# Optimization experiments

Hardware: AMD Instinct MI355X
Metric: run time of the kernel (lower is better)

Reference implementation:

```python
import jax, jax.numpy as jnp
import numpy as np

B, H, V, A, NANN, DEPTH = 32, 256, 512, 3, 8, 7


def preorder_perm(arity, depth):
    # level-order node index -> pre-order position permutation for a full arity-ary tree
    starts = np.cumsum([0] + [arity ** l for l in range(depth + 1)])
    order = []
    def rec(l, p):
        order.append(int(starts[l] + p))
        if l < depth:
            for c in range(arity):
                rec(l + 1, p * arity + c)
    rec(0, 0)
    return np.asarray(order, dtype=np.int32)


def setup_inputs() -> dict:
    key = jax.random.key(0)
    ks = jax.random.split(key, 12)
    s = 0.05
    return {
        "root_hiddens": jax.random.normal(ks[0], (B, H), jnp.float32),
        "ann_table": jax.random.normal(ks[1], (NANN, H), jnp.float32),
        "w1": jax.random.normal(ks[2], (2 * H, H), jnp.float32) * s,
        "b1": jnp.zeros((2 * H,), jnp.float32),
        "w2": jax.random.normal(ks[3], (V, 2 * H), jnp.float32) * s,
        "b2": jnp.zeros((V,), jnp.float32),
        "gru_w_ih": jax.random.normal(ks[4], (A, 3 * H, H), jnp.float32) * s,
        "gru_w_hh": jax.random.normal(ks[5], (A, 3 * H, H), jnp.float32) * s,
        "gru_b_ih": jnp.zeros((A, 3 * H), jnp.float32),
        "gru_b_hh": jnp.zeros((A, 3 * H), jnp.float32),
        "ann_ids": jax.random.randint(ks[6], (B,), 0, NANN, jnp.int32),
        "depth": DEPTH,
    }


def _forward(root_hiddens, ann_table, w1, b1, w2, b2,
             gru_w_ih, gru_w_hh, gru_b_ih, gru_b_hh, ann_ids, depth):
    b, h = root_hiddens.shape
    arity = gru_w_ih.shape[0]
    x = ann_table[ann_ids]                                   # [B,H] annotation embedding (GRU input at every node)
    # input-side gates are constant across the whole tree: precompute once
    gx = jnp.einsum('bh,agh->bag', x, gru_w_ih) + gru_b_ih   # [B,A,3H]
    xr, xz, xn = jnp.split(gx, 3, axis=-1)                   # each [B,A,H]

    hid = root_hiddens[:, None, :]                           # [B,1,H]
    levels = [hid]
    for _ in range(depth):
        gh = jnp.einsum('bnh,agh->bnag', hid, gru_w_hh) + gru_b_hh  # [B,n,A,3H]
        hr, hz, hn = jnp.split(gh, 3, axis=-1)
        r = jax.nn.sigmoid(xr[:, None] + hr)
        z = jax.nn.sigmoid(xz[:, None] + hz)
        n = jnp.tanh(xn[:, None] + r * hn)
        new_h = (1.0 - z) * n + z * hid[:, :, None, :]       # [B,n,A,H]
        hid = new_h.reshape(b, -1, h)                        # child c of node p -> p*A+c
        levels.append(hid)

    all_h = jnp.concatenate(levels, axis=1)                  # [B,N,H] level-order
    mid = jax.nn.sigmoid(jnp.einsum('bnh,oh->bno', all_h, w1) + b1)
    prod = jnp.einsum('bno,vo->bnv', mid, w2) + b2           # [B,N,V]
    perm = jnp.asarray(preorder_perm(arity, depth))
    return jnp.transpose(prod[:, perm, :], (1, 0, 2))        # [N,B,V] (seq-first, like pad_sequence)


def reference(root_hiddens, ann_table, w1, b1, w2, b2,
              gru_w_ih, gru_w_hh, gru_b_ih, gru_b_hh, ann_ids, depth):
    return _forward(root_hiddens, ann_table, w1, b1, w2, b2,
                    gru_w_ih, gru_w_hh, gru_b_ih, gru_b_hh, ann_ids, depth)
```

## Files before the change

kernel.cpp:

```cpp
#include <hip/hip_runtime.h>
#include <hip/hip_bf16.h>
#include <stdint.h>
#include <stddef.h>

#define NB 32
#define NH 256
#define NMID 512
#define NV 512
#define NA 3
#define NDEPTH 7
#define NNODES 3280
#define NG 2304
#define MROWS (NNODES * NB)
#define HM 64

typedef __attribute__((ext_vector_type(8))) short bf16x8;
typedef __attribute__((ext_vector_type(4))) float f32x4;

__device__ __forceinline__ unsigned short f2bf(float x) {
    union { float f; unsigned u; } v; v.f = x;
    unsigned r = v.u + 0x7fffu + ((v.u >> 16) & 1u);
    return (unsigned short)(r >> 16);
}
__device__ __forceinline__ float bf2f(unsigned short u) {
    union { unsigned u; float f; } v; v.u = ((unsigned)u) << 16;
    return v.f;
}
__device__ __forceinline__ float sigm(float x) { return 1.0f / (1.0f + __expf(-x)); }
__device__ __forceinline__ float tanh_(float x) {
    x = fminf(fmaxf(x, -15.0f), 15.0f);
    float e = __expf(2.0f * x);
    return (e - 1.0f) / (e + 1.0f);
}
__device__ __forceinline__ f32x4 splat4(float s) { f32x4 v = {s, s, s, s}; return v; }

__global__ void cast_weights(const float* __restrict__ whh, const float* __restrict__ w1,
                             const float* __restrict__ w2,
                             unsigned short* __restrict__ whh_b,
                             unsigned short* __restrict__ w1_b,
                             unsigned short* __restrict__ w2_b) {
    const int n_whh = NG * NH;
    const int n_w1  = NMID * NH;
    const int n_w2  = NV * NMID;
    const int total = n_whh + n_w1 + n_w2;
    for (int i = blockIdx.x * blockDim.x + threadIdx.x; i < total;
         i += gridDim.x * blockDim.x) {
        if (i < n_whh) whh_b[i] = f2bf(whh[i]);
        else if (i < n_whh + n_w1) w1_b[i - n_whh] = f2bf(w1[i - n_whh]);
        else w2_b[i - n_whh - n_w1] = f2bf(w2[i - n_whh - n_w1]);
    }
}

__global__ void gx_kernel(const float* __restrict__ ann_table, const int* __restrict__ ann_ids,
                          const float* __restrict__ w_ih, const float* __restrict__ b_ih,
                          float* __restrict__ gx_t) {
    int gw = blockIdx.x * (blockDim.x >> 6) + (threadIdx.x >> 6);
    int lane = threadIdx.x & 63;
    if (gw >= NB * NG) return;
    int b = gw / NG;
    int col = gw - b * NG;
    const float* xr = ann_table + (size_t)ann_ids[b] * NH;
    const float* wr = w_ih + (size_t)col * NH;
    float4 xv = *(const float4*)(xr + lane * 4);
    float4 wv = *(const float4*)(wr + lane * 4);
    float s = xv.x * wv.x + xv.y * wv.y + xv.z * wv.z + xv.w * wv.w;
    #pragma unroll
    for (int off = 32; off; off >>= 1) s += __shfl_down(s, off);
    if (lane == 0) gx_t[(size_t)col * NB + b] = s + b_ih[col];
}

__global__ void init_root(const float* __restrict__ root, unsigned short* __restrict__ hid_b) {
    int i = blockIdx.x * blockDim.x + threadIdx.x;
    if (i < NB * NH) hid_b[i] = f2bf(root[i]);
}

__global__ void posmap_kernel(int* __restrict__ posmap) {
    int n = blockIdx.x * blockDim.x + threadIdx.x;
    if (n >= NNODES) return;
    int start = 0, cnt = 1, l = 0;
    while (n >= start + cnt) { start += cnt; cnt *= 3; l++; }
    int p = n - start;
    int pw = 1;
    for (int j = 0; j < l - 1; j++) pw *= 3;
    int pos = 0;
    for (int k = 1; k <= l; k++) {
        int d = (p / pw) % 3;
        int e = NDEPTH - k + 1;
        int p3 = 1; for (int j = 0; j < e; j++) p3 *= 3;
        pos += 1 + d * ((p3 - 1) / 2);
        pw /= 3;
    }
    posmap[n] = pos;
}

template<int NPB>
__global__ __launch_bounds__(512, 4)
void gru_level(const unsigned short* __restrict__ hid_b_in,
               unsigned short* __restrict__ hid_b_out,
               const unsigned short* __restrict__ whh_b,
               const float* __restrict__ b_hh, const float* __restrict__ gx_t,
               int start, int child_start, int cnt) {
    constexpr int M = 32 * NPB;
    __shared__ char a_s[M * 512];

    int tid = threadIdx.x;
    int lane = tid & 63;
    int wv = tid >> 6;
    int lr = lane & 15;
    int kg = (lane >> 4) * 8;
    int rbase = (lane >> 4) * 4;
    int nrel0 = blockIdx.x * NPB;
    size_t prow0 = (size_t)(start + nrel0) * NB;

    for (int c = tid; c < M * 32; c += 512) {
        int row = c >> 5;
        int coloff = (c & 31) * 8;
        bf16x8 v = *(const bf16x8*)(hid_b_in + (prow0 + row) * NH + coloff);
        *(bf16x8*)(a_s + ((row * 512 + coloff * 2) ^ ((row & 15) << 4))) = v;
    }
    __syncthreads();

    int Gb = (blockIdx.y * 8 + wv) * 16;
    int a = Gb >> 8;
    int colh = (Gb & 255) + lr;
    int gcol = a * 768 + colh;
    const unsigned short* bptr = whh_b + (size_t)(a * 512 + Gb + lr) * NH + kg;

    float bhr = b_hh[gcol], bhz = b_hh[gcol + 256], bhn = b_hh[gcol + 512];

    f32x4 acc[3][2 * NPB];
    #pragma unroll
    for (int g = 0; g < 2; ++g) {
        f32x4 gr = *(const f32x4*)(gx_t + (size_t)gcol * NB + g * 16 + rbase);
        f32x4 gz = *(const f32x4*)(gx_t + (size_t)(gcol + 256) * NB + g * 16 + rbase);
        #pragma unroll
        for (int mi = g; mi < 2 * NPB; mi += 2) {
            acc[0][mi] = gr + splat4(bhr);
            acc[1][mi] = gz + splat4(bhz);
            acc[2][mi] = splat4(bhn);
        }
    }

    bf16x8 bcur[3];
    #pragma unroll
    for (int t = 0; t < 3; ++t) bcur[t] = *(const bf16x8*)(bptr + t * 256 * NH);
    #pragma unroll
    for (int k0 = 0; k0 < NH; k0 += 32) {
        bf16x8 bnxt[3];
        if (k0 + 32 < NH) {
            #pragma unroll
            for (int t = 0; t < 3; ++t) bnxt[t] = *(const bf16x8*)(bptr + t * 256 * NH + k0 + 32);
        }
        bf16x8 af[2 * NPB];
        #pragma unroll
        for (int mi = 0; mi < 2 * NPB; ++mi) {
            int row = mi * 16 + lr;
            af[mi] = *(const bf16x8*)(a_s + ((row * 512 + (k0 + kg) * 2) ^ ((row & 15) << 4)));
        }
        #pragma unroll
        for (int t = 0; t < 3; ++t)
            #pragma unroll
            for (int mi = 0; mi < 2 * NPB; ++mi)
                acc[t][mi] = __builtin_amdgcn_mfma_f32_16x16x32_bf16(af[mi], bcur[t], acc[t][mi], 0, 0, 0);
        if (k0 + 32 < NH) {
            #pragma unroll
            for (int t = 0; t < 3; ++t) bcur[t] = bnxt[t];
        }
    }

    f32x4 gxn[2];
    #pragma unroll
    for (int g = 0; g < 2; ++g)
        gxn[g] = *(const f32x4*)(gx_t + (size_t)(gcol + 512) * NB + g * 16 + rbase);
    #pragma unroll
    for (int mi = 0; mi < 2 * NPB; ++mi) {
        #pragma unroll
        for (int j = 0; j < 4; ++j) {
            int row = mi * 16 + rbase + j;
            int ns = row >> 5;
            int b = row & 31;
            if (nrel0 + ns < cnt) {
                float r = sigm(acc[0][mi][j]);
                float z = sigm(acc[1][mi][j]);
                float nn = tanh_(gxn[mi & 1][j] + r * acc[2][mi][j]);
                unsigned short hpu = *(const unsigned short*)(a_s + ((row * 512 + colh * 2) ^ ((row & 15) << 4)));
                float hnew = (1.0f - z) * nn + z * bf2f(hpu);
                size_t crow = ((size_t)(child_start + (nrel0 + ns) * 3 + a)) * NB + b;
                hid_b_out[crow * NH + colh] = f2bf(hnew);
            }
        }
    }
}

__global__ __launch_bounds__(512, 4)
void head_fused(const unsigned short* __restrict__ hid_b,
                const unsigned short* __restrict__ w1_b, const float* __restrict__ b1,
                const unsigned short* __restrict__ w2_b, const float* __restrict__ b2,
                const int* __restrict__ posmap, float* __restrict__ out) {
    __shared__ char smem[HM * NMID * 2];

    int tid = threadIdx.x;
    int lane = tid & 63;
    int wv = tid >> 6;
    int mbase = blockIdx.x * HM;
    int lr = lane & 15;
    int kg = (lane >> 4) * 8;
    int rbase = (lane >> 4) * 4;
    int n0w = wv * 64;

    for (int c = tid; c < HM * 32; c += 512) {
        int row = c >> 5;
        int coloff = (c & 31) * 8;
        bf16x8 v = *(const bf16x8*)(hid_b + ((size_t)(mbase + row)) * NH + coloff);
        *(bf16x8*)(smem + ((row * 512 + coloff * 2) ^ ((row & 15) << 4))) = v;
    }
    __syncthreads();

    f32x4 acc[4][4];
    #pragma unroll
    for (int mi = 0; mi < 4; ++mi)
        #pragma unroll
        for (int ni = 0; ni < 4; ++ni) acc[mi][ni] = (f32x4){0.f, 0.f, 0.f, 0.f};

    {
        const unsigned short* bbase = w1_b + ((size_t)(n0w + lr)) * NH + kg;
        bf16x8 bcur[4];
        #pragma unroll
        for (int ni = 0; ni < 4; ++ni) bcur[ni] = *(const bf16x8*)(bbase + ni * 16 * NH);
        #pragma unroll
        for (int k0 = 0; k0 < NH; k0 += 32) {
            bf16x8 bnxt[4];
            if (k0 + 32 < NH) {
                #pragma unroll
                for (int ni = 0; ni < 4; ++ni) bnxt[ni] = *(const bf16x8*)(bbase + ni * 16 * NH + k0 + 32);
            }
            bf16x8 af[4];
            #pragma unroll
            for (int mi = 0; mi < 4; ++mi) {
                int row = mi * 16 + lr;
                af[mi] = *(const bf16x8*)(smem + ((row * 512 + (k0 + kg) * 2) ^ ((row & 15) << 4)));
            }
            #pragma unroll
            for (int mi = 0; mi < 4; ++mi)
                #pragma unroll
                for (int ni = 0; ni < 4; ++ni)
                    acc[mi][ni] = __builtin_amdgcn_mfma_f32_16x16x32_bf16(af[mi], bcur[ni], acc[mi][ni], 0, 0, 0);
            if (k0 + 32 < NH) {
                #pragma unroll
                for (int ni = 0; ni < 4; ++ni) bcur[ni] = bnxt[ni];
            }
        }
    }
    __syncthreads();

    #pragma unroll
    for (int mi = 0; mi < 4; ++mi)
        #pragma unroll
        for (int ni = 0; ni < 4; ++ni) {
            int col = n0w + ni * 16 + lr;
            float bv = b1[col];
            #pragma unroll
            for (int j = 0; j < 4; ++j) {
                int row = mi * 16 + rbase + j;
                float v = sigm(acc[mi][ni][j] + bv);
                *(unsigned short*)(smem + ((row * 1024 + col * 2) ^ ((row & 15) << 4))) = f2bf(v);
            }
        }
    __syncthreads();

    #pragma unroll
    for (int mi = 0; mi < 4; ++mi)
        #pragma unroll
        for (int ni = 0; ni < 4; ++ni) acc[mi][ni] = (f32x4){0.f, 0.f, 0.f, 0.f};
    {
        const unsigned short* bbase = w2_b + ((size_t)(n0w + lr)) * NMID + kg;
        bf16x8 bcur[4];
        #pragma unroll
        for (int ni = 0; ni < 4; ++ni) bcur[ni] = *(const bf16x8*)(bbase + ni * 16 * NMID);
        #pragma unroll
        for (int k0 = 0; k0 < NMID; k0 += 32) {
            bf16x8 bnxt[4];
            if (k0 + 32 < NMID) {
                #pragma unroll
                for (int ni = 0; ni < 4; ++ni) bnxt[ni] = *(const bf16x8*)(bbase + ni * 16 * NMID + k0 + 32);
            }
            bf16x8 af[4];
            #pragma unroll
            for (int mi = 0; mi < 4; ++mi) {
                int row = mi * 16 + lr;
                af[mi] = *(const bf16x8*)(smem + ((row * 1024 + (k0 + kg) * 2) ^ ((row & 15) << 4)));
            }
            #pragma unroll
            for (int mi = 0; mi < 4; ++mi)
                #pragma unroll
                for (int ni = 0; ni < 4; ++ni)
                    acc[mi][ni] = __builtin_amdgcn_mfma_f32_16x16x32_bf16(af[mi], bcur[ni], acc[mi][ni], 0, 0, 0);
            if (k0 + 32 < NMID) {
                #pragma unroll
                for (int ni = 0; ni < 4; ++ni) bcur[ni] = bnxt[ni];
            }
        }
    }
    #pragma unroll
    for (int mi = 0; mi < 4; ++mi)
        #pragma unroll
        for (int ni = 0; ni < 4; ++ni) {
            int col = n0w + ni * 16 + lr;
            float bv = b2[col];
            #pragma unroll
            for (int j = 0; j < 4; ++j) {
                int row = mbase + mi * 16 + rbase + j;
                int b = row & 31;
                int node = row >> 5;
                int pos = posmap[node];
                out[((size_t)pos * NB + b) * NV + col] = acc[mi][ni][j] + bv;
            }
        }
}

extern "C" void kernel_launch(void* const* d_in, const int* in_sizes, int n_in,
                              void* d_out, int out_size, void* d_ws, size_t ws_size,
                              hipStream_t stream) {
    const float* root      = (const float*)d_in[0];
    const float* ann_table = (const float*)d_in[1];
    const float* w1        = (const float*)d_in[2];
    const float* b1        = (const float*)d_in[3];
    const float* w2        = (const float*)d_in[4];
    const float* b2        = (const float*)d_in[5];
    const float* w_ih      = (const float*)d_in[6];
    const float* w_hh      = (const float*)d_in[7];
    const float* b_ih      = (const float*)d_in[8];
    const float* b_hh      = (const float*)d_in[9];
    const int*   ann_ids   = (const int*)d_in[10];

    uint8_t* ws = (uint8_t*)d_ws;
    unsigned short* whh_b = (unsigned short*)ws; ws += (size_t)NG * NH * 2;
    unsigned short* w1_b  = (unsigned short*)ws; ws += (size_t)NMID * NH * 2;
    unsigned short* w2_b  = (unsigned short*)ws; ws += (size_t)NV * NMID * 2;
    float* gx_t           = (float*)ws;          ws += (size_t)NB * NG * 4;
    int* posmap           = (int*)ws;            ws += (size_t)NNODES * 4;
    unsigned short* hid_b = (unsigned short*)ws; ws += (size_t)NNODES * NB * NH * 2;

    cast_weights<<<512, 256, 0, stream>>>(w_hh, w1, w2, whh_b, w1_b, w2_b);
    gx_kernel<<<(NB * NG) / 4, 256, 0, stream>>>(ann_table, ann_ids, w_ih, b_ih, gx_t);
    init_root<<<(NB * NH + 255) / 256, 256, 0, stream>>>(root, hid_b);
    posmap_kernel<<<(NNODES + 255) / 256, 256, 0, stream>>>(posmap);

    int start = 0, cnt = 1;
    for (int l = 0; l < NDEPTH; ++l) {
        int child_start = start + cnt;
        if (cnt >= 128) {
            gru_level<2><<<dim3((cnt + 1) / 2, 6), 512, 0, stream>>>(
                hid_b, hid_b, whh_b, b_hh, gx_t, start, child_start, cnt);
        } else {
            gru_level<1><<<dim3(cnt, 6), 512, 0, stream>>>(
                hid_b, hid_b, whh_b, b_hh, gx_t, start, child_start, cnt);
        }
        start = child_start; cnt *= 3;
    }
    head_fused<<<MROWS / HM, 512, 0, stream>>>(hid_b, w1_b, b1, w2_b, b2, posmap, (float*)d_out);
}
```

Before: 373.9 us.

## Shrink head tile to one node per block and retune GRU node batching

The head kernel now processes 32 rows (one tree node) per block instead of 64. That lets it look up posmap once per block and write contiguous output rows, and it drops the register double-buffering of weight fragments in favour of direct loads. Occupancy hints change (head 6, GRU 2), and large GRU levels batch 4 nodes per block starting from level size 243. The smaller head tile doubles weight-fragment global traffic per output row and loses software prefetch, in exchange for higher occupancy and cheaper output addressing.

```diff
diff --git a/kernel.cpp b/kernel.cpp
--- a/kernel.cpp
+++ b/kernel.cpp
@@ -12,7 +12,7 @@
 #define NNODES 3280
 #define NG 2304
 #define MROWS (NNODES * NB)
-#define HM 64
+#define HM 32
 
 typedef __attribute__((ext_vector_type(8))) short bf16x8;
 typedef __attribute__((ext_vector_type(4))) float f32x4;
@@ -94,7 +94,7 @@
 }
 
 template<int NPB>
-__global__ __launch_bounds__(512, 4)
+__global__ __launch_bounds__(512, 2)
 void gru_level(const unsigned short* __restrict__ hid_b_in,
                unsigned short* __restrict__ hid_b_out,
                const unsigned short* __restrict__ whh_b,
@@ -192,7 +192,7 @@
     }
 }
 
-__global__ __launch_bounds__(512, 4)
+__global__ __launch_bounds__(512, 6)
 void head_fused(const unsigned short* __restrict__ hid_b,
                 const unsigned short* __restrict__ w1_b, const float* __restrict__ b1,
                 const unsigned short* __restrict__ w2_b, const float* __restrict__ b2,
@@ -216,45 +216,35 @@
     }
     __syncthreads();
 
-    f32x4 acc[4][4];
-    #pragma unroll
-    for (int mi = 0; mi < 4; ++mi)
+    f32x4 acc[2][4];
+    #pragma unroll
+    for (int mi = 0; mi < 2; ++mi)
         #pragma unroll
         for (int ni = 0; ni < 4; ++ni) acc[mi][ni] = (f32x4){0.f, 0.f, 0.f, 0.f};
 
     {
         const unsigned short* bbase = w1_b + ((size_t)(n0w + lr)) * NH + kg;
-        bf16x8 bcur[4];
-        #pragma unroll
-        for (int ni = 0; ni < 4; ++ni) bcur[ni] = *(const bf16x8*)(bbase + ni * 16 * NH);
         #pragma unroll
         for (int k0 = 0; k0 < NH; k0 += 32) {
-            bf16x8 bnxt[4];
-            if (k0 + 32 < NH) {
-                #pragma unroll
-                for (int ni = 0; ni < 4; ++ni) bnxt[ni] = *(const bf16x8*)(bbase + ni * 16 * NH + k0 + 32);
-            }
-            bf16x8 af[4];
-            #pragma unroll
-            for (int mi = 0; mi < 4; ++mi) {
+            bf16x8 af[2], bfr[4];
+            #pragma unroll
+            for (int ni = 0; ni < 4; ++ni) bfr[ni] = *(const bf16x8*)(bbase + ni * 16 * NH + k0);
+            #pragma unroll
+            for (int mi = 0; mi < 2; ++mi) {
                 int row = mi * 16 + lr;
                 af[mi] = *(const bf16x8*)(smem + ((row * 512 + (k0 + kg) * 2) ^ ((row & 15) << 4)));
             }
             #pragma unroll
-            for (int mi = 0; mi < 4; ++mi)
+            for (int mi = 0; mi < 2; ++mi)
                 #pragma unroll
                 for (int ni = 0; ni < 4; ++ni)
-                    acc[mi][ni] = __builtin_amdgcn_mfma_f32_16x16x32_bf16(af[mi], bcur[ni], acc[mi][ni], 0, 0, 0);
-            if (k0 + 32 < NH) {
-                #pragma unroll
-                for (int ni = 0; ni < 4; ++ni) bcur[ni] = bnxt[ni];
-            }
+                    acc[mi][ni] = __builtin_amdgcn_mfma_f32_16x16x32_bf16(af[mi], bfr[ni], acc[mi][ni], 0, 0, 0);
         }
     }
     __syncthreads();
 
     #pragma unroll
-    for (int mi = 0; mi < 4; ++mi)
+    for (int mi = 0; mi < 2; ++mi)
         #pragma unroll
         for (int ni = 0; ni < 4; ++ni) {
             int col = n0w + ni * 16 + lr;
@@ -269,51 +259,40 @@
     __syncthreads();
 
     #pragma unroll
-    for (int mi = 0; mi < 4; ++mi)
+    for (int mi = 0; mi < 2; ++mi)
         #pragma unroll
         for (int ni = 0; ni < 4; ++ni) acc[mi][ni] = (f32x4){0.f, 0.f, 0.f, 0.f};
     {
         const unsigned short* bbase = w2_b + ((size_t)(n0w + lr)) * NMID + kg;
-        bf16x8 bcur[4];
-        #pragma unroll
-        for (int ni = 0; ni < 4; ++ni) bcur[ni] = *(const bf16x8*)(bbase + ni * 16 * NMID);
         #pragma unroll
         for (int k0 = 0; k0 < NMID; k0 += 32) {
-            bf16x8 bnxt[4];
-            if (k0 + 32 < NMID) {
-                #pragma unroll
-                for (int ni = 0; ni < 4; ++ni) bnxt[ni] = *(const bf16x8*)(bbase + ni * 16 * NMID + k0 + 32);
-            }
-            bf16x8 af[4];
-            #pragma unroll
-            for (int mi = 0; mi < 4; ++mi) {
+            bf16x8 af[2], bfr[4];
+            #pragma unroll
+            for (int ni = 0; ni < 4; ++ni) bfr[ni] = *(const bf16x8*)(bbase + ni * 16 * NMID + k0);
+            #pragma unroll
+            for (int mi = 0; mi < 2; ++mi) {
                 int row = mi * 16 + lr;
                 af[mi] = *(const bf16x8*)(smem + ((row * 1024 + (k0 + kg) * 2) ^ ((row & 15) << 4)));
             }
             #pragma unroll
-            for (int mi = 0; mi < 4; ++mi)
+            for (int mi = 0; mi < 2; ++mi)
                 #pragma unroll
                 for (int ni = 0; ni < 4; ++ni)
-                    acc[mi][ni] = __builtin_amdgcn_mfma_f32_16x16x32_bf16(af[mi], bcur[ni], acc[mi][ni], 0, 0, 0);
-            if (k0 + 32 < NMID) {
-                #pragma unroll
-                for (int ni = 0; ni < 4; ++ni) bcur[ni] = bnxt[ni];
-            }
-        }
-    }
-    #pragma unroll
-    for (int mi = 0; mi < 4; ++mi)
+                    acc[mi][ni] = __builtin_amdgcn_mfma_f32_16x16x32_bf16(af[mi], bfr[ni], acc[mi][ni], 0, 0, 0);
+        }
+    }
+    int pos = posmap[blockIdx.x];
+    float* orow = out + (size_t)pos * NB * NV;
+    #pragma unroll
+    for (int mi = 0; mi < 2; ++mi)
         #pragma unroll
         for (int ni = 0; ni < 4; ++ni) {
             int col = n0w + ni * 16 + lr;
             float bv = b2[col];
             #pragma unroll
             for (int j = 0; j < 4; ++j) {
-                int row = mbase + mi * 16 + rbase + j;
-                int b = row & 31;
-                int node = row >> 5;
-                int pos = posmap[node];
-                out[((size_t)pos * NB + b) * NV + col] = acc[mi][ni][j] + bv;
+                int b = mi * 16 + rbase + j;
+                orow[(size_t)b * NV + col] = acc[mi][ni][j] + bv;
             }
         }
 }
@@ -349,8 +328,8 @@
     int start = 0, cnt = 1;
     for (int l = 0; l < NDEPTH; ++l) {
         int child_start = start + cnt;
-        if (cnt >= 128) {
-            gru_level<2><<<dim3((cnt + 1) / 2, 6), 512, 0, stream>>>(
+        if (cnt >= 243) {
+            gru_level<4><<<dim3((cnt + 3) / 4, 6), 512, 0, stream>>>(
                 hid_b, hid_b, whh_b, b_hh, gx_t, start, child_start, cnt);
         } else {
             gru_level<1><<<dim3(cnt, 6), 512, 0, stream>>>(
@@ -358,5 +337,5 @@
         }
         start = child_start; cnt *= 3;
     }
-    head_fused<<<MROWS / HM, 512, 0, stream>>>(hid_b, w1_b, b1, w2_b, b2, posmap, (float*)d_out);
-}
+    head_fused<<<NNODES, 512, 0, stream>>>(hid_b, w1_b, b1, w2_b, b2, posmap, (float*)d_out);
+}
```

Result: slower. 499.9 us (+33.7%).

## Deepen weight prefetch in head GEMMs, relax launch bounds, batch more nodes per GRU block

Applied to the files above, without the earlier changes.

The head kernel's weight-fragment prefetch goes from one k-step ahead to two. The first w2 fragments are now issued before the barrier and sigmoid epilogue, so their latency overlaps the stage-1 epilogue. Launch bounds drop to 2 waves/SIMD for gru_level and 3 for head_fused, freeing more registers for the deeper buffers. The GRU level kernel now processes 4 parent nodes per block for levels with at least 243 nodes, which reuses W_hh across more rows but shrinks the grid and doubles shared memory per block.

```diff
diff --git a/kernel.cpp b/kernel.cpp
--- a/kernel.cpp
+++ b/kernel.cpp
@@ -94,7 +94,7 @@
 }
 
 template<int NPB>
-__global__ __launch_bounds__(512, 4)
+__global__ __launch_bounds__(512, 2)
 void gru_level(const unsigned short* __restrict__ hid_b_in,
                unsigned short* __restrict__ hid_b_out,
                const unsigned short* __restrict__ whh_b,
@@ -192,7 +192,7 @@
     }
 }
 
-__global__ __launch_bounds__(512, 4)
+__global__ __launch_bounds__(512, 3)
 void head_fused(const unsigned short* __restrict__ hid_b,
                 const unsigned short* __restrict__ w1_b, const float* __restrict__ b1,
                 const unsigned short* __restrict__ w2_b, const float* __restrict__ b2,
@@ -224,33 +224,45 @@
 
     {
         const unsigned short* bbase = w1_b + ((size_t)(n0w + lr)) * NH + kg;
-        bf16x8 bcur[4];
-        #pragma unroll
-        for (int ni = 0; ni < 4; ++ni) bcur[ni] = *(const bf16x8*)(bbase + ni * 16 * NH);
-        #pragma unroll
-        for (int k0 = 0; k0 < NH; k0 += 32) {
-            bf16x8 bnxt[4];
-            if (k0 + 32 < NH) {
-                #pragma unroll
-                for (int ni = 0; ni < 4; ++ni) bnxt[ni] = *(const bf16x8*)(bbase + ni * 16 * NH + k0 + 32);
-            }
+        bf16x8 b0[4], b1v[4];
+        #pragma unroll
+        for (int ni = 0; ni < 4; ++ni) b0[ni] = *(const bf16x8*)(bbase + ni * 16 * NH);
+        #pragma unroll
+        for (int ni = 0; ni < 4; ++ni) b1v[ni] = *(const bf16x8*)(bbase + ni * 16 * NH + 32);
+        #pragma unroll
+        for (int kk = 0; kk < 8; ++kk) {
+            int k0 = kk * 32;
             bf16x8 af[4];
             #pragma unroll
             for (int mi = 0; mi < 4; ++mi) {
                 int row = mi * 16 + lr;
                 af[mi] = *(const bf16x8*)(smem + ((row * 512 + (k0 + kg) * 2) ^ ((row & 15) << 4)));
             }
+            bf16x8 bn[4];
+            if (kk + 2 < 8) {
+                #pragma unroll
+                for (int ni = 0; ni < 4; ++ni) bn[ni] = *(const bf16x8*)(bbase + ni * 16 * NH + k0 + 64);
+            }
             #pragma unroll
             for (int mi = 0; mi < 4; ++mi)
                 #pragma unroll
                 for (int ni = 0; ni < 4; ++ni)
-                    acc[mi][ni] = __builtin_amdgcn_mfma_f32_16x16x32_bf16(af[mi], bcur[ni], acc[mi][ni], 0, 0, 0);
-            if (k0 + 32 < NH) {
-                #pragma unroll
-                for (int ni = 0; ni < 4; ++ni) bcur[ni] = bnxt[ni];
-            }
-        }
-    }
+                    acc[mi][ni] = __builtin_amdgcn_mfma_f32_16x16x32_bf16(af[mi], b0[ni], acc[mi][ni], 0, 0, 0);
+            #pragma unroll
+            for (int ni = 0; ni < 4; ++ni) {
+                b0[ni] = b1v[ni];
+                if (kk + 2 < 8) b1v[ni] = bn[ni];
+            }
+        }
+    }
+
+    const unsigned short* bbase2 = w2_b + ((size_t)(n0w + lr)) * NMID + kg;
+    bf16x8 p0[4], p1[4];
+    #pragma unroll
+    for (int ni = 0; ni < 4; ++ni) p0[ni] = *(const bf16x8*)(bbase2 + ni * 16 * NMID);
+    #pragma unroll
+    for (int ni = 0; ni < 4; ++ni) p1[ni] = *(const bf16x8*)(bbase2 + ni * 16 * NMID + 32);
+
     __syncthreads();
 
     #pragma unroll
@@ -273,31 +285,29 @@
         #pragma unroll
         for (int ni = 0; ni < 4; ++ni) acc[mi][ni] = (f32x4){0.f, 0.f, 0.f, 0.f};
     {
-        const unsigned short* bbase = w2_b + ((size_t)(n0w + lr)) * NMID + kg;
-        bf16x8 bcur[4];
-        #pragma unroll
-        for (int ni = 0; ni < 4; ++ni) bcur[ni] = *(const bf16x8*)(bbase + ni * 16 * NMID);
-        #pragma unroll
-        for (int k0 = 0; k0 < NMID; k0 += 32) {
-            bf16x8 bnxt[4];
-            if (k0 + 32 < NMID) {
-                #pragma unroll
-                for (int ni = 0; ni < 4; ++ni) bnxt[ni] = *(const bf16x8*)(bbase + ni * 16 * NMID + k0 + 32);
-            }
+        #pragma unroll
+        for (int kk = 0; kk < 16; ++kk) {
+            int k0 = kk * 32;
             bf16x8 af[4];
             #pragma unroll
             for (int mi = 0; mi < 4; ++mi) {
                 int row = mi * 16 + lr;
                 af[mi] = *(const bf16x8*)(smem + ((row * 1024 + (k0 + kg) * 2) ^ ((row & 15) << 4)));
             }
+            bf16x8 bn[4];
+            if (kk + 2 < 16) {
+                #pragma unroll
+                for (int ni = 0; ni < 4; ++ni) bn[ni] = *(const bf16x8*)(bbase2 + ni * 16 * NMID + k0 + 64);
+            }
             #pragma unroll
             for (int mi = 0; mi < 4; ++mi)
                 #pragma unroll
                 for (int ni = 0; ni < 4; ++ni)
-                    acc[mi][ni] = __builtin_amdgcn_mfma_f32_16x16x32_bf16(af[mi], bcur[ni], acc[mi][ni], 0, 0, 0);
-            if (k0 + 32 < NMID) {
-                #pragma unroll
-                for (int ni = 0; ni < 4; ++ni) bcur[ni] = bnxt[ni];
+                    acc[mi][ni] = __builtin_amdgcn_mfma_f32_16x16x32_bf16(af[mi], p0[ni], acc[mi][ni], 0, 0, 0);
+            #pragma unroll
+            for (int ni = 0; ni < 4; ++ni) {
+                p0[ni] = p1[ni];
+                if (kk + 2 < 16) p1[ni] = bn[ni];
             }
         }
     }
@@ -349,8 +359,8 @@
     int start = 0, cnt = 1;
     for (int l = 0; l < NDEPTH; ++l) {
         int child_start = start + cnt;
-        if (cnt >= 128) {
-            gru_level<2><<<dim3((cnt + 1) / 2, 6), 512, 0, stream>>>(
+        if (cnt >= 243) {
+            gru_level<4><<<dim3((cnt + 3) / 4, 6), 512, 0, stream>>>(
                 hid_b, hid_b, whh_b, b_hh, gx_t, start, child_start, cnt);
         } else {
             gru_level<1><<<dim3(cnt, 6), 512, 0, stream>>>(
```

New measurement: 423.3 us. +13.2%, slower.
